# Kernel optimization log

Measured on AMD Instinct MI355X. Metric: run time of the kernel, lower is better.

Reference implementation:

```python
import jax, jax.numpy as jnp
import numpy as np

ALPHA_LINK = 2.0  # alpha_link from __init__


def setup_inputs() -> dict:
    key = jax.random.key(0)
    B, C = 65536, 1000
    k0, k1, k2, k3 = jax.random.split(key, 4)
    y_pred = jax.random.normal(k0, (B, C), dtype=jnp.float32)
    y_true = jax.random.randint(k1, (B,), 0, C)
    weight = jax.random.uniform(k2, (C,), dtype=jnp.float32)
    # dense boolean class-link matrix: link_matrix[gt, pred] == True means pred is linked to gt
    link_matrix = jax.random.randint(k3, (C, C), 0, 2).astype(jnp.bool_)
    return {"y_pred": y_pred, "y_true": y_true, "weight": weight, "link_matrix": link_matrix}


def reference(y_pred, y_true, weight, link_matrix):
    # per-sample penalty: alpha_link if (pred != gt) and pred is linked to gt, else 1
    pred = jnp.argmax(y_pred, axis=1)                      # [B]
    linked = link_matrix[y_true, pred]                     # [B] bool gather
    penalty = jnp.where((pred != y_true) & linked, ALPHA_LINK, 1.0)  # [B]

    # weighted cross-entropy, reduction='none' semantics: loss_i = weight[y_i] * nll_i
    logp = jax.nn.log_softmax(y_pred, axis=1)              # [B, C]
    nll = -jnp.take_along_axis(logp, y_true[:, None], axis=1)[:, 0]  # [B]
    ce = weight[y_true] * nll                              # [B]

    return jnp.mean(penalty * ce)
```

## Files before the change

kernel.cpp:

```cpp
#include <hip/hip_runtime.h>
#include <math.h>


#define B_SAMPLES 65536
#define C_CLASSES 1000
#define C4 250

__global__ __launch_bounds__(256) void lce_kernel(
    const float* __restrict__ y_pred,
    const int* __restrict__ y_true,
    const float* __restrict__ weight,
    const int* __restrict__ link,
    float* __restrict__ out)
{
    const int lane = threadIdx.x & 63;
    const int wave = threadIdx.x >> 6;
    const int gwave = blockIdx.x * 4 + wave;
    const int nwaves = gridDim.x * 4;

    float local = 0.0f;

    for (int s = gwave; s < B_SAMPLES; s += nwaves) {
        const float4* row = (const float4*)(y_pred + (size_t)s * C_CLASSES);

        float4 v[4];
        #pragma unroll
        for (int it = 0; it < 4; ++it) {
            int idx = it * 64 + lane;
            if (idx < C4) {
                v[it] = row[idx];
            } else {
                v[it] = make_float4(-INFINITY, -INFINITY, -INFINITY, -INFINITY);
            }
        }

        float m = -INFINITY;
        int am = 0;
        #pragma unroll
        for (int it = 0; it < 4; ++it) {
            const float* p = (const float*)&v[it];
            #pragma unroll
            for (int j = 0; j < 4; ++j) {
                float x = p[j];
                int col = (it * 64 + lane) * 4 + j;
                if (x > m) { m = x; am = col; }
            }
        }

        float sum = 0.0f;
        #pragma unroll
        for (int it = 0; it < 4; ++it) {
            const float* p = (const float*)&v[it];
            #pragma unroll
            for (int j = 0; j < 4; ++j) {
                sum += __expf(p[j] - m);
            }
        }

        #pragma unroll
        for (int off = 32; off > 0; off >>= 1) {
            float om  = __shfl_xor(m, off, 64);
            float os  = __shfl_xor(sum, off, 64);
            int   oam = __shfl_xor(am, off, 64);
            float M = fmaxf(m, om);
            sum = sum * __expf(m - M) + os * __expf(om - M);
            am = (om > m || (om == m && oam < am)) ? oam : am;
            m = M;
        }

        if (lane == 0) {
            int t = y_true[s];
            float xt = y_pred[(size_t)s * C_CLASSES + t];
            float nll = m + __logf(sum) - xt;
            float pen = (am != t && link[(size_t)t * C_CLASSES + am] != 0)
                            ? 2.0f : 1.0f;
            local += pen * weight[t] * nll;
        }
    }

    __shared__ float wsum[4];
    if (lane == 0) wsum[wave] = local;
    __syncthreads();
    if (threadIdx.x == 0) {
        float total = (wsum[0] + wsum[1] + wsum[2] + wsum[3]) * (1.0f / B_SAMPLES);
        atomicAdd(out, total);
    }
}

extern "C" void kernel_launch(void* const* d_in, const int* in_sizes, int n_in,
                              void* d_out, int out_size, void* d_ws, size_t ws_size,
                              hipStream_t stream) {
    const float* y_pred = (const float*)d_in[0];
    const int* y_true   = (const int*)d_in[1];
    const float* weight = (const float*)d_in[2];
    const int* link     = (const int*)d_in[3];
    float* out          = (float*)d_out;

    hipMemsetAsync(out, 0, sizeof(float), stream);

    lce_kernel<<<2048, 256, 0, stream>>>(y_pred, y_true, weight, link, out);
}
```

Measured before the change: 364.2 us.

## Process two rows per wave, hoist scalar loads, split max and sum reductions

Each wave now handles two sample rows per iteration. This doubles the loads in flight, and the per-sample label, target logit and weight are loaded up front as wave-uniform values. The online-softmax shuffle merge is replaced by a max/argmax butterfly reduction, then exponentials computed with the global max, then a plain sum reduction. This removes the exp calls inside the shuffle loop. The cost is higher register pressure, and the loop assumes sample counts divide evenly by twice the wave count.

New measurement: 366.5 us. Within noise of the previous version (+0.6%).

```diff
diff --git a/kernel.cpp b/kernel.cpp
--- a/kernel.cpp
+++ b/kernel.cpp
@@ -20,62 +20,85 @@
 
     float local = 0.0f;
 
-    for (int s = gwave; s < B_SAMPLES; s += nwaves) {
-        const float4* row = (const float4*)(y_pred + (size_t)s * C_CLASSES);
+    for (int s0 = gwave; s0 < B_SAMPLES; s0 += 2 * nwaves) {
+        const int sA = __builtin_amdgcn_readfirstlane(s0);
+        const int sB = sA + nwaves;
 
-        float4 v[4];
+        const int tA = y_true[sA];
+        const int tB = y_true[sB];
+        const float xtA = y_pred[(size_t)sA * C_CLASSES + tA];
+        const float xtB = y_pred[(size_t)sB * C_CLASSES + tB];
+        const float wgA = weight[tA];
+        const float wgB = weight[tB];
+
+        const float4* rowA = (const float4*)(y_pred + (size_t)sA * C_CLASSES);
+        const float4* rowB = (const float4*)(y_pred + (size_t)sB * C_CLASSES);
+
+        float4 vA[4], vB[4];
         #pragma unroll
         for (int it = 0; it < 4; ++it) {
             int idx = it * 64 + lane;
-            if (idx < C4) {
-                v[it] = row[idx];
-            } else {
-                v[it] = make_float4(-INFINITY, -INFINITY, -INFINITY, -INFINITY);
-            }
+            if (idx < C4) vA[it] = rowA[idx];
+            else vA[it] = make_float4(-INFINITY, -INFINITY, -INFINITY, -INFINITY);
+        }
+        #pragma unroll
+        for (int it = 0; it < 4; ++it) {
+            int idx = it * 64 + lane;
+            if (idx < C4) vB[it] = rowB[idx];
+            else vB[it] = make_float4(-INFINITY, -INFINITY, -INFINITY, -INFINITY);
         }
 
-        float m = -INFINITY;
-        int am = 0;
+        float mA = -INFINITY, mB = -INFINITY;
+        int amA = 0, amB = 0;
         #pragma unroll
         for (int it = 0; it < 4; ++it) {
-            const float* p = (const float*)&v[it];
+            const float* pA = (const float*)&vA[it];
+            const float* pB = (const float*)&vB[it];
             #pragma unroll
             for (int j = 0; j < 4; ++j) {
-                float x = p[j];
                 int col = (it * 64 + lane) * 4 + j;
-                if (x > m) { m = x; am = col; }
-            }
-        }
-
-        float sum = 0.0f;
-        #pragma unroll
-        for (int it = 0; it < 4; ++it) {
-            const float* p = (const float*)&v[it];
-            #pragma unroll
-            for (int j = 0; j < 4; ++j) {
-                sum += __expf(p[j] - m);
+                if (pA[j] > mA) { mA = pA[j]; amA = col; }
+                if (pB[j] > mB) { mB = pB[j]; amB = col; }
             }
         }
 
         #pragma unroll
         for (int off = 32; off > 0; off >>= 1) {
-            float om  = __shfl_xor(m, off, 64);
-            float os  = __shfl_xor(sum, off, 64);
-            int   oam = __shfl_xor(am, off, 64);
-            float M = fmaxf(m, om);
-            sum = sum * __expf(m - M) + os * __expf(om - M);
-            am = (om > m || (om == m && oam < am)) ? oam : am;
-            m = M;
+            float omA = __shfl_xor(mA, off, 64);
+            int   oaA = __shfl_xor(amA, off, 64);
+            float omB = __shfl_xor(mB, off, 64);
+            int   oaB = __shfl_xor(amB, off, 64);
+            bool tkA = (omA > mA) || (omA == mA && oaA < amA);
+            bool tkB = (omB > mB) || (omB == mB && oaB < amB);
+            mA = tkA ? omA : mA;  amA = tkA ? oaA : amA;
+            mB = tkB ? omB : mB;  amB = tkB ? oaB : amB;
         }
 
-        if (lane == 0) {
-            int t = y_true[s];
-            float xt = y_pred[(size_t)s * C_CLASSES + t];
-            float nll = m + __logf(sum) - xt;
-            float pen = (am != t && link[(size_t)t * C_CLASSES + am] != 0)
-                            ? 2.0f : 1.0f;
-            local += pen * weight[t] * nll;
+        float sumA = 0.0f, sumB = 0.0f;
+        #pragma unroll
+        for (int it = 0; it < 4; ++it) {
+            const float* pA = (const float*)&vA[it];
+            const float* pB = (const float*)&vB[it];
+            #pragma unroll
+            for (int j = 0; j < 4; ++j) {
+                sumA += __expf(pA[j] - mA);
+                sumB += __expf(pB[j] - mB);
+            }
         }
+
+        #pragma unroll
+        for (int off = 32; off > 0; off >>= 1) {
+            sumA += __shfl_xor(sumA, off, 64);
+            sumB += __shfl_xor(sumB, off, 64);
+        }
+
+        int amAu = __builtin_amdgcn_readfirstlane(amA);
+        int amBu = __builtin_amdgcn_readfirstlane(amB);
+        float nllA = mA + __logf(sumA) - xtA;
+        float nllB = mB + __logf(sumB) - xtB;
+        float penA = (amAu != tA && link[(size_t)tA * C_CLASSES + amAu] != 0) ? 2.0f : 1.0f;
+        float penB = (amBu != tB && link[(size_t)tB * C_CLASSES + amBu] != 0) ? 2.0f : 1.0f;
+        local += penA * wgA * nllA + penB * wgB * nllB;
     }
 
     __shared__ float wsum[4];
```
